# Kernel optimization log

Hardware: AMD Instinct MI355X
Metric: run time of the kernel (lower is better)

Reference implementation:

```python
import jax, jax.numpy as jnp
import numpy as np

B, S, E, H, L, D = 16, 512, 512, 8, 3, 64
OBS, ACT, NA = 128, 16, 8
KAPPAS = jnp.asarray(1.0 - 2.0 ** (-5.0 - np.arange(H)), jnp.float32)  # per-head retention decay, decay_scaling_factor=1.0
INV_SQRT_D = 1.0 / float(np.sqrt(D))


def rmsnorm(x, w, eps=1e-6):
    return x * jax.lax.rsqrt(jnp.mean(x * x, -1, keepdims=True) + eps) * w


def swiglu(x, wg, wp):
    return jax.nn.silu(x @ wg) * (x @ wp)


def sin_pe(ts, dim):
    # sinusoidal timestep positional encoding, ts: (B,S) float -> (B,S,dim)
    half = dim // 2
    freqs = jnp.exp(-np.log(10000.0) * jnp.arange(half, dtype=jnp.float32) / half)
    ang = ts[..., None] * freqs
    return jnp.concatenate([jnp.sin(ang), jnp.cos(ang)], -1)


def retention(xk, xq, xv, h0, ts, wq, wk, wv, wo, masked):
    # chunkwise multi-scale retention with cross-chunk recurrent state h0: (B,H,D,D)
    b, s, e = xq.shape
    pe = sin_pe(ts, e)
    q = ((xq + pe) @ wq).reshape(b, s, H, D).transpose(0, 2, 1, 3)            # (B,H,S,D)
    k = ((xk + pe) @ wk).reshape(b, s, H, D).transpose(0, 2, 1, 3) * INV_SQRT_D
    v = ((xv + pe) @ wv).reshape(b, s, H, D).transpose(0, 2, 1, 3)
    lk = jnp.log(KAPPAS)                                                      # (H,)
    diff = ts[:, None, :, None] - ts[:, None, None, :]                        # (B,1,S,S) timestep gaps
    if masked:
        idx = jnp.arange(s)
        allow = (diff > 0) | ((diff == 0) & (idx[:, None] >= idx[None, :]))
        dmat = jnp.where(allow, jnp.exp(lk[None, :, None, None] * diff), 0.0)
    else:
        dmat = jnp.exp(lk[None, :, None, None] * jnp.abs(diff))
    scores = jnp.einsum('bhnd,bhmd->bhnm', q, k) * dmat                       # decay-masked scores
    xi = jnp.exp(lk[None, :, None] * (ts[:, None, :] + 1.0))                  # (B,H,S) cross-chunk decay
    out = jnp.einsum('bhnm,bhmd->bhnd', scores, v) + jnp.einsum('bhnd,bhde->bhne', q, h0) * xi[..., None]
    tmax = ts.max(-1)                                                         # (B,)
    wst = jnp.exp(lk[None, :, None] * (tmax[:, None, None] - ts[:, None, :]))  # (B,H,S)
    h_new = jnp.exp(lk[None, :] * (tmax[:, None] + 1.0))[..., None, None] * h0 \
        + jnp.einsum('bhm,bhmd,bhme->bhde', wst, k, v)
    out = out.transpose(0, 2, 1, 3).reshape(b, s, e) @ wo
    return out, h_new


def _forward(obs, action, enc_hs, dec_hs1, dec_hs2, step_count, params):
    (eoln, eow, eln, ewq, ewk, ewv, ewo, eln1, eln2, efg, efp,
     ehw1, ehb1, ehln, ehw2, ehb2,
     daw, dln, dwq1, dwk1, dwv1, dwo1, dwq2, dwk2, dwv2, dwo2,
     dln1, dln2, dln3, dfg, dfp,
     dhw1, dhb1, dhln, dhw2, dhb2) = params
    ts = step_count.astype(jnp.float32)
    # ---- Encoder ----
    obs_rep = jax.nn.gelu(rmsnorm(obs, eoln) @ eow)
    enc_new = []
    for i in range(L):
        x = rmsnorm(obs_rep, eln)
        ret, hn = retention(x, x, x, enc_hs[:, i], ts, ewq[i], ewk[i], ewv[i], ewo[i], masked=False)
        x = rmsnorm(x + ret, eln1[i])
        obs_rep = rmsnorm(x + swiglu(x, efg[i], efp[i]), eln2[i])
        enc_new.append(hn)
    value = rmsnorm(jax.nn.gelu(obs_rep @ ehw1 + ehb1), ehln) @ ehw2 + ehb2
    # ---- Decoder ----
    x = rmsnorm(jax.nn.gelu(action @ daw), dln)
    d1_new, d2_new = [], []
    for i in range(L):
        ret, h1 = retention(x, x, x, dec_hs1[:, i], ts, dwq1[i], dwk1[i], dwv1[i], dwo1[i], masked=True)
        r = rmsnorm(x + ret, dln1[i])
        ret2, h2 = retention(r, obs_rep, r, dec_hs2[:, i], ts, dwq2[i], dwk2[i], dwv2[i], dwo2[i], masked=True)
        y = rmsnorm(obs_rep + ret2, dln2[i])
        x = rmsnorm(y + swiglu(y, dfg[i], dfp[i]), dln3[i])
        d1_new.append(h1)
        d2_new.append(h2)
    logits = rmsnorm(jax.nn.gelu(x @ dhw1 + dhb1), dhln) @ dhw2 + dhb2
    return value, logits, jnp.stack(enc_new, 1), jnp.stack(d1_new, 1), jnp.stack(d2_new, 1)


def setup_inputs():
    key = jax.random.key(0)
    ki = iter(jax.random.split(key, 50))
    def w(shape, s=0.02):
        return jax.random.normal(next(ki), shape, jnp.float32) * s
    inp = {
        'obs': jax.random.normal(next(ki), (B, S, OBS), jnp.float32),
        'action': jax.random.uniform(next(ki), (B, S, ACT + 1), jnp.float32),
        'enc_hs': jnp.zeros((B, L, H, D, D), jnp.float32),
        'dec_hs1': jnp.zeros((B, L, H, D, D), jnp.float32),
        'dec_hs2': jnp.zeros((B, L, H, D, D), jnp.float32),
        'step_count': jnp.broadcast_to(jnp.arange(S, dtype=jnp.int32) // NA, (B, S)),
        'enc_obs_ln_w': jnp.ones((OBS,), jnp.float32),
        'enc_obs_w': w((OBS, E)),
        'enc_ln_w': jnp.ones((E,), jnp.float32),
        'enc_wq': w((L, E, E)), 'enc_wk': w((L, E, E)), 'enc_wv': w((L, E, E)), 'enc_wo': w((L, E, E)),
        'enc_ln1_w': jnp.ones((L, E), jnp.float32), 'enc_ln2_w': jnp.ones((L, E), jnp.float32),
        'enc_ffn_gate': w((L, E, E)), 'enc_ffn_proj': w((L, E, E)),
        'enc_head_w1': w((E, E)), 'enc_head_b1': jnp.zeros((E,), jnp.float32),
        'enc_head_ln': jnp.ones((E,), jnp.float32),
        'enc_head_w2': w((E, 1)), 'enc_head_b2': jnp.zeros((1,), jnp.float32),
        'dec_act_w': w((ACT + 1, E)), 'dec_ln_w': jnp.ones((E,), jnp.float32),
        'dec_wq1': w((L, E, E)), 'dec_wk1': w((L, E, E)), 'dec_wv1': w((L, E, E)), 'dec_wo1': w((L, E, E)),
        'dec_wq2': w((L, E, E)), 'dec_wk2': w((L, E, E)), 'dec_wv2': w((L, E, E)), 'dec_wo2': w((L, E, E)),
        'dec_ln1_w': jnp.ones((L, E), jnp.float32), 'dec_ln2_w': jnp.ones((L, E), jnp.float32),
        'dec_ln3_w': jnp.ones((L, E), jnp.float32),
        'dec_ffn_gate': w((L, E, E)), 'dec_ffn_proj': w((L, E, E)),
        'dec_head_w1': w((E, E)), 'dec_head_b1': jnp.zeros((E,), jnp.float32),
        'dec_head_ln': jnp.ones((E,), jnp.float32),
        'dec_head_w2': w((E, ACT)), 'dec_head_b2': jnp.zeros((ACT,), jnp.float32),
    }
    return inp


def reference(obs, action, enc_hs, dec_hs1, dec_hs2, step_count, enc_obs_ln_w, enc_obs_w, enc_ln_w, enc_wq, enc_wk, enc_wv, enc_wo, enc_ln1_w, enc_ln2_w, enc_ffn_gate, enc_ffn_proj, enc_head_w1, enc_head_b1, enc_head_ln, enc_head_w2, enc_head_b2, dec_act_w, dec_ln_w, dec_wq1, dec_wk1, dec_wv1, dec_wo1, dec_wq2, dec_wk2, dec_wv2, dec_wo2, dec_ln1_w, dec_ln2_w, dec_ln3_w, dec_ffn_gate, dec_ffn_proj, dec_head_w1, dec_head_b1, dec_head_ln, dec_head_w2, dec_head_b2):
    params = (enc_obs_ln_w, enc_obs_w, enc_ln_w, enc_wq, enc_wk, enc_wv, enc_wo, enc_ln1_w, enc_ln2_w, enc_ffn_gate, enc_ffn_proj, enc_head_w1, enc_head_b1, enc_head_ln, enc_head_w2, enc_head_b2, dec_act_w, dec_ln_w, dec_wq1, dec_wk1, dec_wv1, dec_wo1, dec_wq2, dec_wk2, dec_wv2, dec_wo2, dec_ln1_w, dec_ln2_w, dec_ln3_w, dec_ffn_gate, dec_ffn_proj, dec_head_w1, dec_head_b1, dec_head_ln, dec_head_w2, dec_head_b2)
    return _forward(obs, action, enc_hs, dec_hs1, dec_hs2, step_count, params)
```

## Files before the change

kernel.cpp:

```cpp
#include <hip/hip_runtime.h>
#include <hip/hip_bf16.h>
#include <math.h>

typedef __attribute__((ext_vector_type(8))) short short8;
typedef __attribute__((ext_vector_type(4))) short short4v;
typedef __attribute__((ext_vector_type(4))) float f32x4;

#define BB 16
#define SS 512
#define EE 512
#define HH 8
#define DH 64
#define LL 3
#define MM (BB*SS)
#define OBSD 128
#define ACTD 17
#define INV_SQRT_D 0.125f

#define ACT_NONE 0
#define ACT_GELU 1

#define NORM_PLAIN 0
#define NORM_ADD 1

// ... 42 lines not shown
}

struct TP50 { const float* s[50]; unsigned short* d[50]; };
__global__ __launch_bounds__(256) void wtpose_batch_kernel(TP50 tp)
{
  __shared__ float t[32][33];
  const float* src = tp.s[blockIdx.z];
  unsigned short* dst = tp.d[blockIdx.z];
  const int gx = blockIdx.x, gy = blockIdx.y;
  const int tx = threadIdx.x, ty = threadIdx.y;
  #pragma unroll
  for (int i = 0; i < 4; ++i){
    int k = gx*32 + ty + i*8, n = gy*32 + tx;
    t[ty+i*8][tx] = src[(size_t)k*EE + n];
  }
  __syncthreads();
  #pragma unroll
  for (int i = 0; i < 4; ++i){
    int k = gx*32 + tx, n = gy*32 + ty + i*8;
    dst[(size_t)n*EE + k] = f2bs(t[tx][ty+i*8]);
  }
}

template<int SW>
__global__ __launch_bounds__(256) void gemm_b_kernel(
    const unsigned short* __restrict__ A, const unsigned short* __restrict__ Wt,
    const unsigned short* __restrict__ Wt2,
    const float* __restrict__ bias, float* __restrict__ C,
    unsigned short* __restrict__ Cb,
    int Kpad, float scale, int act,
    const int* __restrict__ tsi, float dsign,
    unsigned short* __restrict__ lo_n,
    unsigned short* __restrict__ swo)
{
  __shared__ unsigned short As[2][128*64];
  __shared__ unsigned short Bs[2][64*64];
  __shared__ unsigned short Bs2[SW ? 2 : 1][SW ? 64*64 : 8];
  const int bm = blockIdx.y*128, bn = blockIdx.x*64;
  const int tid = threadIdx.x, lane = tid & 63, wv = tid >> 6;
  const int wr = wv >> 1, wc = wv & 1;
  const int l16 = lane & 15, quad = lane >> 4;

  f32x4 acc[4][2], acc2[SW ? 4 : 1][SW ? 2 : 1];
  #pragma unroll
  for (int i=0;i<4;i++){ acc[i][0]=(f32x4)(0.f); acc[i][1]=(f32x4)(0.f); }
  if (SW){
    #pragma unroll
    for (int i=0;i<4;i++){ acc2[i][0]=(f32x4)(0.f); acc2[i][1]=(f32x4)(0.f); }
  }

  const int sg = lane >> 3;
  const int lg = (lane & 7) ^ sg;
  size_t aoff[4], boff[2];
  #pragma unroll
  for (int i=0;i<4;i++)
    aoff[i] = (size_t)(bm + (wv*4+i)*8 + sg)*Kpad + lg*8;
  #pragma unroll
  for (int i=0;i<2;i++)
    boff[i] = (size_t)(bn + (wv*2+i)*8 + sg)*Kpad + lg*8;

  const int swz = (l16 & 7) << 3;

  auto STAGE = [&](int buf, int t){
    const int k0 = t*64;
    #pragma unroll
    for (int i=0;i<4;i++)
      gl16(A + aoff[i] + k0, (char*)&As[buf][0] + ((wv*4+i) << 10));
    #pragma unroll
    for (int i=0;i<2;i++)
      gl16(Wt + boff[i] + k0, (char*)&Bs[buf][0] + ((wv*2+i) << 10));
    if (SW){
      #pragma unroll
      for (int i=0;i<2;i++)
        gl16(Wt2 + boff[i] + k0, (char*)&Bs2[buf][0] + ((wv*2+i) << 10));
    }
  };
  auto COMPUTE = [&](int buf){
    short8 af[4][2], bf[2][2];
    #pragma unroll
    for (int mt=0; mt<4; ++mt)
      #pragma unroll
      for (int ks=0; ks<2; ++ks)
        af[mt][ks] = *(const short8*)&As[buf][(wr*64 + mt*16 + l16)*64 + ((ks*32 + quad*8) ^ swz)];
    #pragma unroll
    for (int nt=0; nt<2; ++nt)
      #pragma unroll
      for (int ks=0; ks<2; ++ks)
        bf[nt][ks] = *(const short8*)&Bs[buf][(wc*32 + nt*16 + l16)*64 + ((ks*32 + quad*8) ^ swz)];
    #pragma unroll
    for (int ks=0; ks<2; ++ks)
      #pragma unroll
      for (int mt=0; mt<4; ++mt)
        #pragma unroll
        for (int nt=0; nt<2; ++nt)
          acc[mt][nt] = __builtin_amdgcn_mfma_f32_16x16x32_bf16(af[mt][ks], bf[nt][ks], acc[mt][nt], 0, 0, 0);
    if (SW){
      short8 bf2[2][2];
      #pragma unroll
      for (int nt=0; nt<2; ++nt)
        #pragma unroll
        for (int ks=0; ks<2; ++ks)
          bf2[nt][ks] = *(const short8*)&Bs2[buf][(wc*32 + nt*16 + l16)*64 + ((ks*32 + quad*8) ^ swz)];
      #pragma unroll
      for (int ks=0; ks<2; ++ks)
        #pragma unroll
        for (int mt=0; mt<4; ++mt)
          #pragma unroll
          for (int nt=0; nt<2; ++nt)
            acc2[mt][nt] = __builtin_amdgcn_mfma_f32_16x16x32_bf16(af[mt][ks], bf2[nt][ks], acc2[mt][nt], 0, 0, 0);
    }
  };

  const int NT = Kpad >> 6;
  STAGE(0, 0);
  PIPE_SYNC;
  int cur = 0;
  for (int t = 0; t < NT; ++t){
    if (t+1 < NT) STAGE(cur^1, t+1);
    COMPUTE(cur);
    if (t+1 < NT) PIPE_SYNC;
    cur ^= 1;
  }

  const float lkh = (!SW && tsi) ? lkappa(bn >> 6) : 0.f;
  #pragma unroll
  for (int mt=0; mt<4; ++mt){
    int rb = bm + wr*64 + mt*16 + quad*4;
    if (SW){
      #pragma unroll
      for (int nt=0; nt<2; ++nt){
        int col = bn + wc*32 + nt*16 + l16;
        #pragma unroll
        for (int j=0;j<4;j++)
          swo[(size_t)(rb+j)*EE + col] = f2bs(silu_f(acc[mt][nt][j])*acc2[mt][nt][j]);
      }
      continue;
    }
    float e0[4];
    if (tsi){
      #pragma unroll
      for (int j=0;j<4;j++) e0[j] = __expf(dsign*lkh*(float)tsi[rb+j]);
    }
    #pragma unroll
    for (int nt=0; nt<2; ++nt){
      int col = bn + wc*32 + nt*16 + l16;
      float bv = bias ? bias[col] : 0.f;
      float vals[4];
      #pragma unroll
      for (int j=0;j<4;j++){
        float v = acc[mt][nt][j]*scale + bv;
        if (act==ACT_GELU) v = gelu_f(v);
        vals[j] = v;
      }
      if (C){
        #pragma unroll
        for (int j=0;j<4;j++) C[(size_t)(rb+j)*EE + col] = vals[j];
      }
      if (Cb){
        #pragma unroll
        for (int j=0;j<4;j++) Cb[(size_t)(rb+j)*EE + col] = f2bs(vals[j]);
      }
      if (tsi){
        #pragma unroll
        for (int j=0;j<4;j++) lo_n[(size_t)(rb+j)*EE + col] = f2bs(vals[j]*e0[j]);
      }
    }
  }
}

template<int ENC>
__global__ __launch_bounds__(256) void gemm_qkv_kernel(
    const unsigned short* __restrict__ A, const unsigned short* __restrict__ Wt,
    int gstart, const int* __restrict__ tsi,
    unsigned short* __restrict__ qlo, unsigned short* __restrict__ qhi,
    unsigned short* __restrict__ klo, unsigned short* __restrict__ kloT,
    unsigned short* __restrict__ khi, unsigned short* __restrict__ khiT,
    unsigned short* __restrict__ vT)
{
  __shared__ unsigned short As[2][128*64];
  __shared__ unsigned short Bs[2][64*64];
  const int bm = blockIdx.y*128, bn = blockIdx.x*64;
  const int tid = threadIdx.x, lane = tid & 63, wv = tid >> 6;
  const int wr = wv >> 1, wc = wv & 1;
  const int l16 = lane & 15, quad = lane >> 4;

  f32x4 acc[4][2];
  #pragma unroll
  for (int i=0;i<4;i++){ acc[i][0]=(f32x4)(0.f); acc[i][1]=(f32x4)(0.f); }

  const int sg = lane >> 3;
  const int lg = (lane & 7) ^ sg;
  size_t aoff[4], boff[2];
  #pragma unroll
  for (int i=0;i<4;i++)
    aoff[i] = (size_t)(bm + (wv*4+i)*8 + sg)*EE + lg*8;
  #pragma unroll
  for (int i=0;i<2;i++)
    boff[i] = (size_t)(bn + (wv*2+i)*8 + sg)*EE + lg*8;

  const int swz = (l16 & 7) << 3;

  auto STAGE = [&](int buf, int t){
    const int k0 = t*64;
    #pragma unroll
    for (int i=0;i<4;i++)
      gl16(A + aoff[i] + k0, (char*)&As[buf][0] + ((wv*4+i) << 10));
    #pragma unroll
    for (int i=0;i<2;i++)
      gl16(Wt + boff[i] + k0, (char*)&Bs[buf][0] + ((wv*2+i) << 10));
  };
  auto COMPUTE = [&](int buf){
    short8 af[4][2], bf[2][2];
    #pragma unroll
    for (int mt=0; mt<4; ++mt)
      #pragma unroll
      for (int ks=0; ks<2; ++ks)
        af[mt][ks] = *(const short8*)&As[buf][(wr*64 + mt*16 + l16)*64 + ((ks*32 + quad*8) ^ swz)];
    #pragma unroll
    for (int nt=0; nt<2; ++nt)
      #pragma unroll
      for (int ks=0; ks<2; ++ks)
        bf[nt][ks] = *(const short8*)&Bs[buf][(wc*32 + nt*16 + l16)*64 + ((ks*32 + quad*8) ^ swz)];
    #pragma unroll
    for (int ks=0; ks<2; ++ks)
      #pragma unroll
      for (int mt=0; mt<4; ++mt)
        #pragma unroll
        for (int nt=0; nt<2; ++nt)
          acc[mt][nt] = __builtin_amdgcn_mfma_f32_16x16x32_bf16(af[mt][ks], bf[nt][ks], acc[mt][nt], 0, 0, 0);
  };

  STAGE(0, 0);
  PIPE_SYNC;
  int cur = 0;
  for (int t = 0; t < 8; ++t){
    if (t+1 < 8) STAGE(cur^1, t+1);
    COMPUTE(cur);
    if (t+1 < 8) PIPE_SYNC;
    cur ^= 1;
  }

  const int group = gstart + (bn >> 9);
  const int coll = bn & 511;
  const int hh = coll >> 6;
  const float lkh = lkappa(hh);
  const float scl = (group == 1) ? INV_SQRT_D : 1.f;
  const float dsg = (group == 1) ? -1.f : 1.f;

  #pragma unroll
  for (int mt=0; mt<4; ++mt){
    int rb = bm + wr*64 + mt*16 + quad*4;
    float e0[4], e1[4];
    if (group < 2){
      #pragma unroll
      for (int j=0;j<4;j++){
        float x = dsg*lkh*(float)tsi[rb+j];
        e0[j] = __expf(x); e1[j] = __expf(-x);
      }
    }
    int bloc = rb >> 9, m0 = rb & 511;
    #pragma unroll
    for (int nt=0; nt<2; ++nt){
      int col = coll + wc*32 + nt*16 + l16;
      int ee = col & 63;
      size_t taddr = (((size_t)bloc*HH + hh)*DH + ee)*SS + m0;
      float vals[4];
      #pragma unroll
      for (int j=0;j<4;j++) vals[j] = acc[mt][nt][j]*scl;
      if (group == 0){
        #pragma unroll
        for (int j=0;j<4;j++) qlo[(size_t)(rb+j)*EE + col] = f2bs(vals[j]*e0[j]);
        if (ENC){
          #pragma unroll
          for (int j=0;j<4;j++) qhi[(size_t)(rb+j)*EE + col] = f2bs(vals[j]*e1[j]);
        }
      } else if (group == 1){
        short4v pk;
        #pragma unroll
        for (int j=0;j<4;j++){
          unsigned short v = f2bs(vals[j]*e0[j]);
          klo[(size_t)(rb+j)*EE + col] = v;
          pk[j] = (short)v;
        }
        *(short4v*)&kloT[taddr] = pk;
        if (ENC){
          short4v pk2;
          #pragma unroll
          for (int j=0;j<4;j++){
            unsigned short v = f2bs(vals[j]*e1[j]);
            khi[(size_t)(rb+j)*EE + col] = v;
            pk2[j] = (short)v;
          }
          *(short4v*)&khiT[taddr] = pk2;
        }
      } else {
        short4v pk;
        #pragma unroll
        for (int j=0;j<4;j++) pk[j] = (short)f2bs(vals[j]);
        *(short4v*)&vT[taddr] = pk;
      }
    }
  }
}

__global__ __launch_bounds__(256) void norm_b_kernel(
    const float* __restrict__ af, const unsigned short* __restrict__ ab,
    const float* __restrict__ res, const unsigned short* __restrict__ resb,
    const float* __restrict__ w, unsigned short* __restrict__ o1,
    unsigned short* __restrict__ o2, const unsigned short* __restrict__ peb,
    int mode)
{
  const int row = blockIdx.x*4 + (threadIdx.x >> 6);
  const int lane = threadIdx.x & 63;
  const size_t base = (size_t)row*EE + lane*8;
  float t[8];
  if (ab){
    short8 av = *(const short8*)&ab[base];
    #pragma unroll
    for (int e=0;e<8;++e) t[e] = bs2f((unsigned short)av[e]);
  } else {
    float4 a0 = *(const float4*)&af[base];
    float4 a1 = *(const float4*)&af[base+4];
    t[0]=a0.x;t[1]=a0.y;t[2]=a0.z;t[3]=a0.w;t[4]=a1.x;t[5]=a1.y;t[6]=a1.z;t[7]=a1.w;
// ... 37 lines not shown
    const float* __restrict__ a, const float* __restrict__ w, unsigned short* __restrict__ o)
{
  const int row = blockIdx.x*4 + (threadIdx.x >> 6);
  const int lane = threadIdx.x & 63;
  const size_t base = (size_t)row*OBSD + lane*2;
  float2 av = *(const float2*)&a[base];
  float ss = av.x*av.x + av.y*av.y;
  #pragma unroll
  for (int off=32;off;off>>=1) ss += __shfl_xor(ss, off);
  float r = 1.f/sqrtf(ss/(float)OBSD + 1e-6f);
  float2 wv2 = *(const float2*)&w[lane*2];
  unsigned int pk = (unsigned int)f2bs(av.x*r*wv2.x) | ((unsigned int)f2bs(av.y*r*wv2.y) << 16);
  *(unsigned int*)&o[base] = pk;
}

__global__ __launch_bounds__(256) void act_embed_kernel(
    const float* __restrict__ a, unsigned short* __restrict__ o)
{
  int idx = blockIdx.x*256 + threadIdx.x;
  int row = idx >> 6, col = idx & 63;
  o[idx] = (col < ACTD) ? f2bs(a[(size_t)row*ACTD + col]) : 0;
}

__global__ __launch_bounds__(256) void wchunk_kernel(
    const unsigned short* __restrict__ kloT, const unsigned short* __restrict__ khiT,
    const unsigned short* __restrict__ vT,
    float* __restrict__ wlo, unsigned short* __restrict__ whi, int enc)
{
  __shared__ unsigned short vsh[64*72];
  __shared__ unsigned short ksh[64*72];
  __shared__ unsigned short ksh2[64*72];
  const int c = blockIdx.x, h = blockIdx.y, b = blockIdx.z;
  const int tid = threadIdx.x, lane = tid & 63, wv = tid >> 6;
  const int quad = lane >> 4, l16 = lane & 15;
  const int mc = c*64;
  {
    const int r = tid >> 2, seg = (tid & 3)*16;
    const unsigned short* vrow = vT   + (((size_t)b*HH + h)*DH + r)*SS + mc + seg;
    const unsigned short* krow = kloT + (((size_t)b*HH + h)*DH + r)*SS + mc + seg;
    #pragma unroll
    for (int i = 0; i < 2; ++i){
      *(short8*)&vsh[r*72 + seg + i*8] = *(const short8*)(vrow + i*8);
      *(short8*)&ksh[r*72 + seg + i*8] = *(const short8*)(krow + i*8);
    }
    if (enc){
      const unsigned short* k2row = khiT + (((size_t)b*HH + h)*DH + r)*SS + mc + seg;
      #pragma unroll
      for (int i = 0; i < 2; ++i)
        *(short8*)&ksh2[r*72 + seg + i*8] = *(const short8*)(k2row + i*8);
    }
  }
  __syncthreads();
  short8 av[2];
  #pragma unroll
  for (int ks=0; ks<2; ++ks)
    av[ks] = *(const short8*)&vsh[(wv*16 + l16)*72 + ks*32 + quad*8];
  f32x4 acc[4];
  #pragma unroll
  for (int dt=0; dt<4; ++dt) acc[dt] = (f32x4)(0.f);
  #pragma unroll
  for (int ks=0; ks<2; ++ks)
    #pragma unroll
    for (int dt=0; dt<4; ++dt){
      short8 kb = *(const short8*)&ksh[(dt*16 + l16)*72 + ks*32 + quad*8];
      acc[dt] = __builtin_amdgcn_mfma_f32_16x16x32_bf16(av[ks], kb, acc[dt], 0, 0, 0);
    }
  size_t obase = (((size_t)b*HH + h)*8 + c)*4096;
  #pragma unroll
  for (int dt=0; dt<4; ++dt)
    #pragma unroll
    for (int j=0;j<4;j++)
      wlo[obase + (size_t)(wv*16 + quad*4 + j)*64 + dt*16 + l16] = acc[dt][j];
  if (enc){
    f32x4 acc2[4];
    #pragma unroll
    for (int dt=0; dt<4; ++dt) acc2[dt] = (f32x4)(0.f);
    #pragma unroll
    for (int ks=0; ks<2; ++ks)
      #pragma unroll
      for (int dt=0; dt<4; ++dt){
        short8 kb = *(const short8*)&ksh2[(dt*16 + l16)*72 + ks*32 + quad*8];
        acc2[dt] = __builtin_amdgcn_mfma_f32_16x16x32_bf16(av[ks], kb, acc2[dt], 0, 0, 0);
      }
    #pragma unroll
    for (int dt=0; dt<4; ++dt)
      #pragma unroll
      for (int j=0;j<4;j++)
        whi[obase + (size_t)(wv*16 + quad*4 + j)*64 + dt*16 + l16] = f2bs(acc2[dt][j]);
  }
}

__global__ __launch_bounds__(256) void wscan_kernel(
    const float* __restrict__ wc, unsigned short* __restrict__ wcum,
    unsigned short* whi,
    const float* __restrict__ h0, const float* __restrict__ tmx,
    float* __restrict__ hnew, int enc)
{
  const int bh = blockIdx.x, b = bh >> 3, h = bh & 7;
  const float lk = lkappa(h);
  const float elk = __expf(lk);
  const float etm = __expf(lk*tmx[b]);
  const size_t wbase = (size_t)bh*8*4096;
  const size_t hbase = (size_t)b*(LL*HH*DH*DH) + (size_t)h*(DH*DH);
  for (int i = 0; i < 16; ++i){
    int p = i*256 + threadIdx.x;
    int e = p >> 6, d = p & 63;
    float acc = elk * h0[hbase + d*64 + e];
    #pragma unroll
    for (int c = 0; c < 8; ++c){
      float reg = wc[wbase + c*4096 + p];
      wcum[wbase + c*4096 + p] = f2bs(acc);
      acc += reg;
    }
    hnew[hbase + d*64 + e] = etm * acc;
    if (enc){
      float a2 = 0.f;
      #pragma unroll
      for (int c = 7; c >= 0; --c){
        float reg = bs2f(whi[wbase + c*4096 + p]);
        whi[wbase + c*4096 + p] = f2bs(a2);
        a2 += reg;
      }
    }
  }
}

template<int ENC>
__global__ __launch_bounds__(256) void retention2_kernel(
    const unsigned short* __restrict__ qlo, const unsigned short* __restrict__ qhi,
    const unsigned short* __restrict__ klo, const unsigned short* __restrict__ khi,
    const unsigned short* __restrict__ vT,
    const unsigned short* __restrict__ wlo, const unsigned short* __restrict__ whi,
    const int* __restrict__ tsi, unsigned short* __restrict__ outp)
{
  __shared__ unsigned short qsh[64*72];
  __shared__ unsigned short wsh[64*72];
  __shared__ unsigned short ksh[64*72];
  __shared__ unsigned short vsh[64*72];
  __shared__ unsigned short qsh2[ENC ? 64*72 : 2];
  __shared__ unsigned short wsh2[ENC ? 64*72 : 2];
  __shared__ float tsf[SS];
  const int b = blockIdx.z, h = blockIdx.y, t = blockIdx.x;
  const int n0 = t*64;
  const int tid = threadIdx.x, lane = tid & 63, wv = tid >> 6;
  const int quad = lane >> 4, l16 = lane & 15;
// ... 257 lines not shown
  const float* dwk1 = (const float*)d_in[25];
  const float* dwv1 = (const float*)d_in[26];
  const float* dwo1 = (const float*)d_in[27];
  const float* dwq2 = (const float*)d_in[28];
  const float* dwk2 = (const float*)d_in[29];
  const float* dwv2 = (const float*)d_in[30];
  const float* dwo2 = (const float*)d_in[31];
  const float* dln1 = (const float*)d_in[32];
  const float* dln2 = (const float*)d_in[33];
  const float* dln3 = (const float*)d_in[34];
  const float* dfg  = (const float*)d_in[35];
  const float* dfp  = (const float*)d_in[36];
  const float* dhw1 = (const float*)d_in[37];
  const float* dhb1 = (const float*)d_in[38];
  const float* dhln = (const float*)d_in[39];
  const float* dhw2 = (const float*)d_in[40];
  const float* dhb2 = (const float*)d_in[41];

  const size_t BUF = (size_t)MM*EE;
  float* wsf  = (float*)d_ws;
  float* f32a = wsf;
  float* f32b = f32a + BUF;
  float* tmx  = f32b + BUF;
  float* wc_lo = f32b;
  unsigned short* wcum_lo = (unsigned short*)f32a;
  unsigned short* wcum_hi = wcum_lo + BUF;
  unsigned short* sw_b    = (unsigned short*)f32b;
  unsigned short* ub = (unsigned short*)(tmx + 64);
  unsigned short* xrep_b    = ub;  ub += BUF;
  unsigned short* xrep_pe_b = ub;  ub += BUF;
  unsigned short* x_b       = ub;  ub += BUF;
  unsigned short* x_pe_b    = ub;  ub += BUF;
  unsigned short* t1_b      = ub;  ub += BUF;
  unsigned short* t1_pe_b   = ub;  ub += BUF;
  unsigned short* peb       = ub;  ub += BUF;
  unsigned short* qlo_b     = ub;  ub += BUF;
  unsigned short* klo_b     = ub;  ub += BUF;
  unsigned short* kloT_b    = ub;  ub += BUF;
  unsigned short* khi_b     = ub;  ub += BUF;
  unsigned short* khiT_b    = ub;  ub += BUF;
  unsigned short* vT_b      = ub;  ub += BUF;
  unsigned short* obs_n     = ub;  ub += (size_t)MM*OBSD;
  unsigned short* act_b     = obs_n;
  unsigned short* qhi_b     = t1_pe_b;
  const size_t W55 = (size_t)EE*EE;
  unsigned short* wts = ub;  ub += 50*W55;
  unsigned short* wt_eow = ub; ub += (size_t)EE*OBSD;
// ... 31 lines not shown
    for (int i=0;i<3;++i){ add(ewq+i*W55); add(ewk+i*W55); add(ewv+i*W55); }
    for (int i=0;i<3;++i) add(ewo+i*W55);
    for (int i=0;i<3;++i) add(efg+i*W55);
    for (int i=0;i<3;++i) add(efp+i*W55);
    add(ehw1);
    for (int i=0;i<3;++i){ add(dwq1+i*W55); add(dwk1+i*W55); add(dwv1+i*W55); }
    for (int i=0;i<3;++i) add(dwo1+i*W55);
    for (int i=0;i<3;++i){ add(dwk2+i*W55); add(dwv2+i*W55); }
    for (int i=0;i<3;++i) add(dwq2+i*W55);
    for (int i=0;i<3;++i) add(dwo2+i*W55);
    for (int i=0;i<3;++i) add(dfg+i*W55);
    for (int i=0;i<3;++i) add(dfp+i*W55);
    add(dhw1);
    wtpose_batch_kernel<<<dim3(16,16,50), dim3(32,8), 0, stream>>>(tp);
  }
  wtpose_kernel<<<dim3(4,16), dim3(32,8), 0, stream>>>(eow, wt_eow, OBSD, OBSD);
  wtpose_kernel<<<dim3(2,16), dim3(32,8), 0, stream>>>(daw, wt_daw, ACTD, 64);

  pe_kernel<<<(MM*EE)/256, 256, 0, stream>>>(stepc, peb);
  tsmax_kernel<<<BB, 256, 0, stream>>>(stepc, tmx);

  auto gemmF = [&](const unsigned short* A, const unsigned short* Wt, const float* bias,
                   float* C, int Kpad, float scale, int act){
    gemm_b_kernel<0><<<dim3(EE/64, MM/128), 256, 0, stream>>>(A, Wt, nullptr, bias, C, nullptr,
        Kpad, scale, act, nullptr, 0.f, nullptr, nullptr);
  };
  auto gemmQ2 = [&](const unsigned short* A, const unsigned short* Wt){
    gemm_b_kernel<0><<<dim3(EE/64, MM/128), 256, 0, stream>>>(A, Wt, nullptr, nullptr, nullptr, nullptr,
        EE, 1.f, ACT_NONE, stepc, 1.f, qlo_b, nullptr);
  };
  auto gemmSW = [&](const unsigned short* A, const unsigned short* Wg, const unsigned short* Wp){
    gemm_b_kernel<1><<<dim3(EE/64, MM/128), 256, 0, stream>>>(A, Wg, Wp, nullptr, nullptr, nullptr,
        EE, 1.f, ACT_NONE, nullptr, 0.f, nullptr, sw_b);
  };
  auto gemmQKV = [&](const unsigned short* A, const unsigned short* Wt, int enc){
    if (enc)
      gemm_qkv_kernel<1><<<dim3(24, MM/128), 256, 0, stream>>>(A, Wt, 0, stepc,
          qlo_b, qhi_b, klo_b, kloT_b, khi_b, khiT_b, vT_b);
    else
      gemm_qkv_kernel<0><<<dim3(24, MM/128), 256, 0, stream>>>(A, Wt, 0, stepc,
          qlo_b, nullptr, klo_b, kloT_b, nullptr, nullptr, vT_b);
  };
  auto gemmKV = [&](const unsigned short* A, const unsigned short* Wt){
    gemm_qkv_kernel<0><<<dim3(16, MM/128), 256, 0, stream>>>(A, Wt, 1, stepc,
        nullptr, nullptr, klo_b, kloT_b, nullptr, nullptr, vT_b);
  };
  auto norm = [&](const float* af, const unsigned short* ab, const float* res,
                  const unsigned short* resb, const float* w,
                  unsigned short* o1, unsigned short* o2, int mode){
    norm_b_kernel<<<MM/4, 256, 0, stream>>>(af, ab, res, resb, w, o1, o2, peb, mode);
  };
  auto retention = [&](const float* h0, float* hnew, unsigned short* o, int enc){
    wchunk_kernel<<<dim3(8, HH, BB), 256, 0, stream>>>(kloT_b, khiT_b, vT_b, wc_lo,
        enc ? wcum_hi : nullptr, enc);
    wscan_kernel<<<BB*HH, 256, 0, stream>>>(wc_lo, wcum_lo, enc ? wcum_hi : nullptr,
        h0, tmx, hnew, enc);
    if (enc)
      retention2_kernel<1><<<dim3(8, HH, BB), 256, 0, stream>>>(
          qlo_b, qhi_b, klo_b, khi_b, vT_b, wcum_lo, wcum_hi, stepc, o);
    else
      retention2_kernel<0><<<dim3(8, HH, BB), 256, 0, stream>>>(
          qlo_b, nullptr, klo_b, nullptr, vT_b, wcum_lo, nullptr, stepc, o);
  };

  norm_obs_kernel<<<MM/4, 256, 0, stream>>>(obs, eoln, obs_n);
  gemmF(obs_n, wt_eow, nullptr, f32a, OBSD, 1.f, ACT_GELU);

  for (int i = 0; i < LL; ++i){
    if (i == 0) norm(f32a, nullptr, nullptr, nullptr, eln, x_b, x_pe_b, NORM_PLAIN);
    else        norm(nullptr, xrep_b, nullptr, nullptr, eln, x_b, x_pe_b, NORM_PLAIN);
    gemmQKV(x_pe_b, wt_eqkv + (size_t)3*i*W55, 1);
    retention(enc_hs + i*HS_L, enc_out + i*HS_L, t1_b, 1);
    gemmF(t1_b, wt_ewo + i*W55, nullptr, f32a, EE, 1.f, ACT_NONE);
    norm(nullptr, x_b, f32a, nullptr, eln1 + i*EE, t1_b, nullptr, NORM_ADD);
    gemmSW(t1_b, wt_efg + i*W55, wt_efp + i*W55);
    norm(nullptr, t1_b, nullptr, sw_b, eln2 + i*EE, xrep_b, xrep_pe_b, NORM_ADD);
  }

  gemmF(xrep_b, wt_ehw1, ehb1, f32a, EE, 1.f, ACT_GELU);
// ... 26 lines not shown
```

Measured before the change: 1.357 ms.

## Use 128x128 GEMM tiles and fuse chunk-state computation with scan

Replaces the 128x64 GEMM kernels with a unified 128x128-tile kernel for the plain, QKV, KV and Q projections, raising operand reuse per block and halving the grid. SwiGLU gets its own kernel. The retention chunk-state GEMM and the prefix scan are merged into one kernel per (head, batch) that loops over chunks sequentially. This removes the fp32 intermediate buffer and one launch, but cuts that stage's parallelism to 128 blocks and adds per-block serial work.

Result: faster. 1.247 ms (-8.1%).

```diff
diff --git a/kernel.cpp b/kernel.cpp
--- a/kernel.cpp
+++ b/kernel.cpp
@@ -88,93 +88,67 @@
   }
 }
 
-template<int SW>
-__global__ __launch_bounds__(256) void gemm_b_kernel(
+template<int MODE, int ENC>
+__global__ __launch_bounds__(256) void gemm128_kernel(
     const unsigned short* __restrict__ A, const unsigned short* __restrict__ Wt,
-    const unsigned short* __restrict__ Wt2,
     const float* __restrict__ bias, float* __restrict__ C,
-    unsigned short* __restrict__ Cb,
     int Kpad, float scale, int act,
-    const int* __restrict__ tsi, float dsign,
-    unsigned short* __restrict__ lo_n,
-    unsigned short* __restrict__ swo)
+    int gstart, const int* __restrict__ tsi,
+    unsigned short* __restrict__ qlo, unsigned short* __restrict__ qhi,
+    unsigned short* __restrict__ klo, unsigned short* __restrict__ kloT,
+    unsigned short* __restrict__ khi, unsigned short* __restrict__ khiT,
+    unsigned short* __restrict__ vT)
 {
   __shared__ unsigned short As[2][128*64];
-  __shared__ unsigned short Bs[2][64*64];
-  __shared__ unsigned short Bs2[SW ? 2 : 1][SW ? 64*64 : 8];
-  const int bm = blockIdx.y*128, bn = blockIdx.x*64;
+  __shared__ unsigned short Bs[2][128*64];
+  const int bm = blockIdx.y*128, bn = blockIdx.x*128;
   const int tid = threadIdx.x, lane = tid & 63, wv = tid >> 6;
   const int wr = wv >> 1, wc = wv & 1;
   const int l16 = lane & 15, quad = lane >> 4;
 
-  f32x4 acc[4][2], acc2[SW ? 4 : 1][SW ? 2 : 1];
-  #pragma unroll
-  for (int i=0;i<4;i++){ acc[i][0]=(f32x4)(0.f); acc[i][1]=(f32x4)(0.f); }
-  if (SW){
-    #pragma unroll
-    for (int i=0;i<4;i++){ acc2[i][0]=(f32x4)(0.f); acc2[i][1]=(f32x4)(0.f); }
-  }
+  f32x4 acc[4][4];
+  #pragma unroll
+  for (int i=0;i<4;i++)
+    #pragma unroll
+    for (int j=0;j<4;j++) acc[i][j]=(f32x4)(0.f);
 
   const int sg = lane >> 3;
   const int lg = (lane & 7) ^ sg;
-  size_t aoff[4], boff[2];
-  #pragma unroll
-  for (int i=0;i<4;i++)
-    aoff[i] = (size_t)(bm + (wv*4+i)*8 + sg)*Kpad + lg*8;
-  #pragma unroll
-  for (int i=0;i<2;i++)
-    boff[i] = (size_t)(bn + (wv*2+i)*8 + sg)*Kpad + lg*8;
-
+  size_t aoff[4], boff[4];
+  #pragma unroll
+  for (int i=0;i<4;i++){
+    aoff[i] = (size_t)(bm + wv*32 + i*8 + sg)*Kpad + lg*8;
+    boff[i] = (size_t)(bn + wv*32 + i*8 + sg)*Kpad + lg*8;
+  }
   const int swz = (l16 & 7) << 3;
 
   auto STAGE = [&](int buf, int t){
     const int k0 = t*64;
     #pragma unroll
-    for (int i=0;i<4;i++)
+    for (int i=0;i<4;i++){
       gl16(A + aoff[i] + k0, (char*)&As[buf][0] + ((wv*4+i) << 10));
-    #pragma unroll
-    for (int i=0;i<2;i++)
-      gl16(Wt + boff[i] + k0, (char*)&Bs[buf][0] + ((wv*2+i) << 10));
-    if (SW){
-      #pragma unroll
-      for (int i=0;i<2;i++)
-        gl16(Wt2 + boff[i] + k0, (char*)&Bs2[buf][0] + ((wv*2+i) << 10));
+      gl16(Wt + boff[i] + k0, (char*)&Bs[buf][0] + ((wv*4+i) << 10));
     }
   };
   auto COMPUTE = [&](int buf){
-    short8 af[4][2], bf[2][2];
+    short8 af[4][2], bf[4][2];
     #pragma unroll
     for (int mt=0; mt<4; ++mt)
       #pragma unroll
       for (int ks=0; ks<2; ++ks)
         af[mt][ks] = *(const short8*)&As[buf][(wr*64 + mt*16 + l16)*64 + ((ks*32 + quad*8) ^ swz)];
     #pragma unroll
-    for (int nt=0; nt<2; ++nt)
+    for (int nt=0; nt<4; ++nt)
       #pragma unroll
       for (int ks=0; ks<2; ++ks)
-        bf[nt][ks] = *(const short8*)&Bs[buf][(wc*32 + nt*16 + l16)*64 + ((ks*32 + quad*8) ^ swz)];
+        bf[nt][ks] = *(const short8*)&Bs[buf][(wc*64 + nt*16 + l16)*64 + ((ks*32 + quad*8) ^ swz)];
     #pragma unroll
     for (int ks=0; ks<2; ++ks)
       #pragma unroll
       for (int mt=0; mt<4; ++mt)
         #pragma unroll
-        for (int nt=0; nt<2; ++nt)
+        for (int nt=0; nt<4; ++nt)
           acc[mt][nt] = __builtin_amdgcn_mfma_f32_16x16x32_bf16(af[mt][ks], bf[nt][ks], acc[mt][nt], 0, 0, 0);
-    if (SW){
-      short8 bf2[2][2];
-      #pragma unroll
-      for (int nt=0; nt<2; ++nt)
-        #pragma unroll
-        for (int ks=0; ks<2; ++ks)
-          bf2[nt][ks] = *(const short8*)&Bs2[buf][(wc*32 + nt*16 + l16)*64 + ((ks*32 + quad*8) ^ swz)];
-      #pragma unroll
-      for (int ks=0; ks<2; ++ks)
-        #pragma unroll
-        for (int mt=0; mt<4; ++mt)
-          #pragma unroll
-          for (int nt=0; nt<2; ++nt)
-            acc2[mt][nt] = __builtin_amdgcn_mfma_f32_16x16x32_bf16(af[mt][ks], bf2[nt][ks], acc2[mt][nt], 0, 0, 0);
-    }
   };
 
   const int NT = Kpad >> 6;
@@ -188,71 +162,103 @@
     cur ^= 1;
   }
 
-  const float lkh = (!SW && tsi) ? lkappa(bn >> 6) : 0.f;
-  #pragma unroll
-  for (int mt=0; mt<4; ++mt){
-    int rb = bm + wr*64 + mt*16 + quad*4;
-    if (SW){
-      #pragma unroll
-      for (int nt=0; nt<2; ++nt){
-        int col = bn + wc*32 + nt*16 + l16;
+  if (MODE == 0){
+    #pragma unroll
+    for (int mt=0; mt<4; ++mt){
+      int rb = bm + wr*64 + mt*16 + quad*4;
+      #pragma unroll
+      for (int nt=0; nt<4; ++nt){
+        int col = bn + wc*64 + nt*16 + l16;
+        float bv = bias ? bias[col] : 0.f;
         #pragma unroll
-        for (int j=0;j<4;j++)
-          swo[(size_t)(rb+j)*EE + col] = f2bs(silu_f(acc[mt][nt][j])*acc2[mt][nt][j]);
-      }
-      continue;
-    }
-    float e0[4];
-    if (tsi){
-      #pragma unroll
-      for (int j=0;j<4;j++) e0[j] = __expf(dsign*lkh*(float)tsi[rb+j]);
-    }
-    #pragma unroll
-    for (int nt=0; nt<2; ++nt){
-      int col = bn + wc*32 + nt*16 + l16;
-      float bv = bias ? bias[col] : 0.f;
-      float vals[4];
-      #pragma unroll
-      for (int j=0;j<4;j++){
-        float v = acc[mt][nt][j]*scale + bv;
-        if (act==ACT_GELU) v = gelu_f(v);
-        vals[j] = v;
-      }
-      if (C){
+        for (int j=0;j<4;j++){
+          float v = acc[mt][nt][j]*scale + bv;
+          if (act==ACT_GELU) v = gelu_f(v);
+          C[(size_t)(rb+j)*EE + col] = v;
+        }
+      }
+    }
+  } else {
+    const int group = gstart + (bn >> 9);
+    const int hh = ((bn & 511) >> 6) + wc;
+    const float lkh = lkappa(hh);
+    const float scl = (group == 1) ? INV_SQRT_D : 1.f;
+    const float dsg = (group == 1) ? -1.f : 1.f;
+    #pragma unroll
+    for (int mt=0; mt<4; ++mt){
+      int rb = bm + wr*64 + mt*16 + quad*4;
+      float e0[4], e1[4];
+      if (group < 2){
         #pragma unroll
-        for (int j=0;j<4;j++) C[(size_t)(rb+j)*EE + col] = vals[j];
-      }
-      if (Cb){
+        for (int j=0;j<4;j++){
+          float x = dsg*lkh*(float)tsi[rb+j];
+          e0[j] = __expf(x); e1[j] = __expf(-x);
+        }
+      }
+      int bloc = rb >> 9, m0 = rb & 511;
+      #pragma unroll
+      for (int nt=0; nt<4; ++nt){
+        int ccol = (bn & 511) + wc*64 + nt*16 + l16;
+        int ee = nt*16 + l16;
+        size_t taddr = (((size_t)bloc*HH + hh)*DH + ee)*SS + m0;
+        float vals[4];
         #pragma unroll
-        for (int j=0;j<4;j++) Cb[(size_t)(rb+j)*EE + col] = f2bs(vals[j]);
-      }
-      if (tsi){
-        #pragma unroll
-        for (int j=0;j<4;j++) lo_n[(size_t)(rb+j)*EE + col] = f2bs(vals[j]*e0[j]);
-      }
-    }
-  }
-}
-
-template<int ENC>
-__global__ __launch_bounds__(256) void gemm_qkv_kernel(
+        for (int j=0;j<4;j++) vals[j] = acc[mt][nt][j]*scl;
+        if (group == 0){
+          #pragma unroll
+          for (int j=0;j<4;j++) qlo[(size_t)(rb+j)*EE + ccol] = f2bs(vals[j]*e0[j]);
+          if (ENC){
+            #pragma unroll
+            for (int j=0;j<4;j++) qhi[(size_t)(rb+j)*EE + ccol] = f2bs(vals[j]*e1[j]);
+          }
+        } else if (group == 1){
+          short4v pk;
+          #pragma unroll
+          for (int j=0;j<4;j++){
+            unsigned short v = f2bs(vals[j]*e0[j]);
+            klo[(size_t)(rb+j)*EE + ccol] = v;
+            pk[j] = (short)v;
+          }
+          *(short4v*)&kloT[taddr] = pk;
+          if (ENC){
+            short4v pk2;
+            #pragma unroll
+            for (int j=0;j<4;j++){
+              unsigned short v = f2bs(vals[j]*e1[j]);
+              khi[(size_t)(rb+j)*EE + ccol] = v;
+              pk2[j] = (short)v;
+            }
+            *(short4v*)&khiT[taddr] = pk2;
+          }
+        } else {
+          short4v pk;
+          #pragma unroll
+          for (int j=0;j<4;j++) pk[j] = (short)f2bs(vals[j]);
+          *(short4v*)&vT[taddr] = pk;
+        }
+      }
+    }
+  }
+}
+
+__global__ __launch_bounds__(256) void gemm_sw_kernel(
     const unsigned short* __restrict__ A, const unsigned short* __restrict__ Wt,
-    int gstart, const int* __restrict__ tsi,
-    unsigned short* __restrict__ qlo, unsigned short* __restrict__ qhi,
-    unsigned short* __restrict__ klo, unsigned short* __restrict__ kloT,
-    unsigned short* __restrict__ khi, unsigned short* __restrict__ khiT,
-    unsigned short* __restrict__ vT)
+    const unsigned short* __restrict__ Wt2, unsigned short* __restrict__ swo)
 {
   __shared__ unsigned short As[2][128*64];
   __shared__ unsigned short Bs[2][64*64];
+  __shared__ unsigned short Bs2[2][64*64];
   const int bm = blockIdx.y*128, bn = blockIdx.x*64;
   const int tid = threadIdx.x, lane = tid & 63, wv = tid >> 6;
   const int wr = wv >> 1, wc = wv & 1;
   const int l16 = lane & 15, quad = lane >> 4;
 
-  f32x4 acc[4][2];
-  #pragma unroll
-  for (int i=0;i<4;i++){ acc[i][0]=(f32x4)(0.f); acc[i][1]=(f32x4)(0.f); }
+  f32x4 acc[4][2], acc2[4][2];
+  #pragma unroll
+  for (int i=0;i<4;i++){
+    acc[i][0]=(f32x4)(0.f); acc[i][1]=(f32x4)(0.f);
+    acc2[i][0]=(f32x4)(0.f); acc2[i][1]=(f32x4)(0.f);
+  }
 
   const int sg = lane >> 3;
   const int lg = (lane & 7) ^ sg;
@@ -272,11 +278,13 @@
     for (int i=0;i<4;i++)
       gl16(A + aoff[i] + k0, (char*)&As[buf][0] + ((wv*4+i) << 10));
     #pragma unroll
-    for (int i=0;i<2;i++)
+    for (int i=0;i<2;i++){
       gl16(Wt + boff[i] + k0, (char*)&Bs[buf][0] + ((wv*2+i) << 10));
+      gl16(Wt2 + boff[i] + k0, (char*)&Bs2[buf][0] + ((wv*2+i) << 10));
+    }
   };
   auto COMPUTE = [&](int buf){
-    short8 af[4][2], bf[2][2];
+    short8 af[4][2], bf[2][2], bf2[2][2];
     #pragma unroll
     for (int mt=0; mt<4; ++mt)
       #pragma unroll
@@ -285,15 +293,19 @@
     #pragma unroll
     for (int nt=0; nt<2; ++nt)
       #pragma unroll
-      for (int ks=0; ks<2; ++ks)
-        bf[nt][ks] = *(const short8*)&Bs[buf][(wc*32 + nt*16 + l16)*64 + ((ks*32 + quad*8) ^ swz)];
+      for (int ks=0; ks<2; ++ks){
+        bf[nt][ks]  = *(const short8*)&Bs[buf][(wc*32 + nt*16 + l16)*64 + ((ks*32 + quad*8) ^ swz)];
+        bf2[nt][ks] = *(const short8*)&Bs2[buf][(wc*32 + nt*16 + l16)*64 + ((ks*32 + quad*8) ^ swz)];
+      }
     #pragma unroll
     for (int ks=0; ks<2; ++ks)
       #pragma unroll
       for (int mt=0; mt<4; ++mt)
         #pragma unroll
-        for (int nt=0; nt<2; ++nt)
-          acc[mt][nt] = __builtin_amdgcn_mfma_f32_16x16x32_bf16(af[mt][ks], bf[nt][ks], acc[mt][nt], 0, 0, 0);
+        for (int nt=0; nt<2; ++nt){
+          acc[mt][nt]  = __builtin_amdgcn_mfma_f32_16x16x32_bf16(af[mt][ks], bf[nt][ks],  acc[mt][nt],  0, 0, 0);
+          acc2[mt][nt] = __builtin_amdgcn_mfma_f32_16x16x32_bf16(af[mt][ks], bf2[nt][ks], acc2[mt][nt], 0, 0, 0);
+        }
   };
 
   STAGE(0, 0);
@@ -306,65 +318,15 @@
     cur ^= 1;
   }
 
-  const int group = gstart + (bn >> 9);
-  const int coll = bn & 511;
-  const int hh = coll >> 6;
-  const float lkh = lkappa(hh);
-  const float scl = (group == 1) ? INV_SQRT_D : 1.f;
-  const float dsg = (group == 1) ? -1.f : 1.f;
-
   #pragma unroll
   for (int mt=0; mt<4; ++mt){
     int rb = bm + wr*64 + mt*16 + quad*4;
-    float e0[4], e1[4];
-    if (group < 2){
-      #pragma unroll
-      for (int j=0;j<4;j++){
-        float x = dsg*lkh*(float)tsi[rb+j];
-        e0[j] = __expf(x); e1[j] = __expf(-x);
-      }
-    }
-    int bloc = rb >> 9, m0 = rb & 511;
     #pragma unroll
     for (int nt=0; nt<2; ++nt){
-      int col = coll + wc*32 + nt*16 + l16;
-      int ee = col & 63;
-      size_t taddr = (((size_t)bloc*HH + hh)*DH + ee)*SS + m0;
-      float vals[4];
-      #pragma unroll
-      for (int j=0;j<4;j++) vals[j] = acc[mt][nt][j]*scl;
-      if (group == 0){
-        #pragma unroll
-        for (int j=0;j<4;j++) qlo[(size_t)(rb+j)*EE + col] = f2bs(vals[j]*e0[j]);
-        if (ENC){
-          #pragma unroll
-          for (int j=0;j<4;j++) qhi[(size_t)(rb+j)*EE + col] = f2bs(vals[j]*e1[j]);
-        }
-      } else if (group == 1){
-        short4v pk;
-        #pragma unroll
-        for (int j=0;j<4;j++){
-          unsigned short v = f2bs(vals[j]*e0[j]);
-          klo[(size_t)(rb+j)*EE + col] = v;
-          pk[j] = (short)v;
-        }
-        *(short4v*)&kloT[taddr] = pk;
-        if (ENC){
-          short4v pk2;
-          #pragma unroll
-          for (int j=0;j<4;j++){
-            unsigned short v = f2bs(vals[j]*e1[j]);
-            khi[(size_t)(rb+j)*EE + col] = v;
-            pk2[j] = (short)v;
-          }
-          *(short4v*)&khiT[taddr] = pk2;
-        }
-      } else {
-        short4v pk;
-        #pragma unroll
-        for (int j=0;j<4;j++) pk[j] = (short)f2bs(vals[j]);
-        *(short4v*)&vT[taddr] = pk;
-      }
+      int col = bn + wc*32 + nt*16 + l16;
+      #pragma unroll
+      for (int j=0;j<4;j++)
+        swo[(size_t)(rb+j)*EE + col] = f2bs(silu_f(acc[mt][nt][j])*acc2[mt][nt][j]);
     }
   }
 }
@@ -448,105 +410,110 @@
   o[idx] = (col < ACTD) ? f2bs(a[(size_t)row*ACTD + col]) : 0;
 }
 
-__global__ __launch_bounds__(256) void wchunk_kernel(
+__global__ __launch_bounds__(256) void wchunkscan_kernel(
     const unsigned short* __restrict__ kloT, const unsigned short* __restrict__ khiT,
     const unsigned short* __restrict__ vT,
-    float* __restrict__ wlo, unsigned short* __restrict__ whi, int enc)
+    const float* __restrict__ h0, const float* __restrict__ tmx,
+    unsigned short* __restrict__ wcum_lo, unsigned short* __restrict__ wcum_hi,
+    float* __restrict__ hnew, int enc)
 {
   __shared__ unsigned short vsh[64*72];
   __shared__ unsigned short ksh[64*72];
-  __shared__ unsigned short ksh2[64*72];
-  const int c = blockIdx.x, h = blockIdx.y, b = blockIdx.z;
+  const int h = blockIdx.x, b = blockIdx.y;
   const int tid = threadIdx.x, lane = tid & 63, wv = tid >> 6;
   const int quad = lane >> 4, l16 = lane & 15;
-  const int mc = c*64;
-  {
-    const int r = tid >> 2, seg = (tid & 3)*16;
-    const unsigned short* vrow = vT   + (((size_t)b*HH + h)*DH + r)*SS + mc + seg;
-    const unsigned short* krow = kloT + (((size_t)b*HH + h)*DH + r)*SS + mc + seg;
-    #pragma unroll
-    for (int i = 0; i < 2; ++i){
-      *(short8*)&vsh[r*72 + seg + i*8] = *(const short8*)(vrow + i*8);
-      *(short8*)&ksh[r*72 + seg + i*8] = *(const short8*)(krow + i*8);
-    }
-    if (enc){
-      const unsigned short* k2row = khiT + (((size_t)b*HH + h)*DH + r)*SS + mc + seg;
-      #pragma unroll
-      for (int i = 0; i < 2; ++i)
-        *(short8*)&ksh2[r*72 + seg + i*8] = *(const short8*)(k2row + i*8);
-    }
-  }
-  __syncthreads();
-  short8 av[2];
-  #pragma unroll
-  for (int ks=0; ks<2; ++ks)
-    av[ks] = *(const short8*)&vsh[(wv*16 + l16)*72 + ks*32 + quad*8];
-  f32x4 acc[4];
-  #pragma unroll
-  for (int dt=0; dt<4; ++dt) acc[dt] = (f32x4)(0.f);
-  #pragma unroll
-  for (int ks=0; ks<2; ++ks)
-    #pragma unroll
-    for (int dt=0; dt<4; ++dt){
-      short8 kb = *(const short8*)&ksh[(dt*16 + l16)*72 + ks*32 + quad*8];
-      acc[dt] = __builtin_amdgcn_mfma_f32_16x16x32_bf16(av[ks], kb, acc[dt], 0, 0, 0);
-    }
-  size_t obase = (((size_t)b*HH + h)*8 + c)*4096;
-  #pragma unroll
-  for (int dt=0; dt<4; ++dt)
-    #pragma unroll
-    for (int j=0;j<4;j++)
-      wlo[obase + (size_t)(wv*16 + quad*4 + j)*64 + dt*16 + l16] = acc[dt][j];
-  if (enc){
-    f32x4 acc2[4];
-    #pragma unroll
-    for (int dt=0; dt<4; ++dt) acc2[dt] = (f32x4)(0.f);
-    #pragma unroll
-    for (int ks=0; ks<2; ++ks)
-      #pragma unroll
-      for (int dt=0; dt<4; ++dt){
-        short8 kb = *(const short8*)&ksh2[(dt*16 + l16)*72 + ks*32 + quad*8];
-        acc2[dt] = __builtin_amdgcn_mfma_f32_16x16x32_bf16(av[ks], kb, acc2[dt], 0, 0, 0);
-      }
-    #pragma unroll
-    for (int dt=0; dt<4; ++dt)
-      #pragma unroll
-      for (int j=0;j<4;j++)
-        whi[obase + (size_t)(wv*16 + quad*4 + j)*64 + dt*16 + l16] = f2bs(acc2[dt][j]);
-  }
-}
-
-__global__ __launch_bounds__(256) void wscan_kernel(
-    const float* __restrict__ wc, unsigned short* __restrict__ wcum,
-    unsigned short* whi,
-    const float* __restrict__ h0, const float* __restrict__ tmx,
-    float* __restrict__ hnew, int enc)
-{
-  const int bh = blockIdx.x, b = bh >> 3, h = bh & 7;
   const float lk = lkappa(h);
   const float elk = __expf(lk);
   const float etm = __expf(lk*tmx[b]);
-  const size_t wbase = (size_t)bh*8*4096;
+  const size_t wbase = ((size_t)b*HH + h)*8*4096;
   const size_t hbase = (size_t)b*(LL*HH*DH*DH) + (size_t)h*(DH*DH);
-  for (int i = 0; i < 16; ++i){
-    int p = i*256 + threadIdx.x;
-    int e = p >> 6, d = p & 63;
-    float acc = elk * h0[hbase + d*64 + e];
-    #pragma unroll
-    for (int c = 0; c < 8; ++c){
-      float reg = wc[wbase + c*4096 + p];
-      wcum[wbase + c*4096 + p] = f2bs(acc);
-      acc += reg;
-    }
-    hnew[hbase + d*64 + e] = etm * acc;
-    if (enc){
-      float a2 = 0.f;
-      #pragma unroll
-      for (int c = 7; c >= 0; --c){
-        float reg = bs2f(whi[wbase + c*4096 + p]);
-        whi[wbase + c*4096 + p] = f2bs(a2);
-        a2 += reg;
-      }
+  const int e0r = wv*16 + quad*4;
+  const int sr = tid >> 2, sseg = (tid & 3)*16;
+
+  f32x4 cum[4];
+  #pragma unroll
+  for (int dt=0; dt<4; ++dt)
+    #pragma unroll
+    for (int j=0;j<4;j++)
+      cum[dt][j] = elk * h0[hbase + (size_t)(dt*16+l16)*64 + e0r + j];
+
+  for (int c = 0; c < 8; ++c){
+    __syncthreads();
+    {
+      const unsigned short* vrow = vT   + (((size_t)b*HH + h)*DH + sr)*SS + c*64 + sseg;
+      const unsigned short* krow = kloT + (((size_t)b*HH + h)*DH + sr)*SS + c*64 + sseg;
+      #pragma unroll
+      for (int i = 0; i < 2; ++i){
+        *(short8*)&vsh[sr*72 + sseg + i*8] = *(const short8*)(vrow + i*8);
+        *(short8*)&ksh[sr*72 + sseg + i*8] = *(const short8*)(krow + i*8);
+      }
+    }
+    __syncthreads();
+    short8 av[2];
+    #pragma unroll
+    for (int ks=0; ks<2; ++ks)
+      av[ks] = *(const short8*)&vsh[(wv*16 + l16)*72 + ks*32 + quad*8];
+    f32x4 acc[4];
+    #pragma unroll
+    for (int dt=0; dt<4; ++dt) acc[dt] = (f32x4)(0.f);
+    #pragma unroll
+    for (int ks=0; ks<2; ++ks)
+      #pragma unroll
+      for (int dt=0; dt<4; ++dt){
+        short8 kb = *(const short8*)&ksh[(dt*16 + l16)*72 + ks*32 + quad*8];
+        acc[dt] = __builtin_amdgcn_mfma_f32_16x16x32_bf16(av[ks], kb, acc[dt], 0, 0, 0);
+      }
+    #pragma unroll
+    for (int dt=0; dt<4; ++dt)
+      #pragma unroll
+      for (int j=0;j<4;j++){
+        wcum_lo[wbase + (size_t)c*4096 + (size_t)(e0r+j)*64 + dt*16 + l16] = f2bs(cum[dt][j]);
+        cum[dt][j] += acc[dt][j];
+      }
+  }
+  #pragma unroll
+  for (int dt=0; dt<4; ++dt)
+    #pragma unroll
+    for (int j=0;j<4;j++)
+      hnew[hbase + (size_t)(dt*16+l16)*64 + e0r + j] = etm * cum[dt][j];
+
+  if (enc){
+    f32x4 suf[4];
+    #pragma unroll
+    for (int dt=0; dt<4; ++dt) suf[dt] = (f32x4)(0.f);
+    for (int c = 7; c >= 0; --c){
+      __syncthreads();
+      {
+        const unsigned short* vrow = vT   + (((size_t)b*HH + h)*DH + sr)*SS + c*64 + sseg;
+        const unsigned short* krow = khiT + (((size_t)b*HH + h)*DH + sr)*SS + c*64 + sseg;
+        #pragma unroll
+        for (int i = 0; i < 2; ++i){
+          *(short8*)&vsh[sr*72 + sseg + i*8] = *(const short8*)(vrow + i*8);
+          *(short8*)&ksh[sr*72 + sseg + i*8] = *(const short8*)(krow + i*8);
+        }
+      }
+      __syncthreads();
+      short8 av[2];
+      #pragma unroll
+      for (int ks=0; ks<2; ++ks)
+        av[ks] = *(const short8*)&vsh[(wv*16 + l16)*72 + ks*32 + quad*8];
+      f32x4 acc[4];
+      #pragma unroll
+      for (int dt=0; dt<4; ++dt) acc[dt] = (f32x4)(0.f);
+      #pragma unroll
+      for (int ks=0; ks<2; ++ks)
+        #pragma unroll
+        for (int dt=0; dt<4; ++dt){
+          short8 kb = *(const short8*)&ksh[(dt*16 + l16)*72 + ks*32 + quad*8];
+          acc[dt] = __builtin_amdgcn_mfma_f32_16x16x32_bf16(av[ks], kb, acc[dt], 0, 0, 0);
+        }
+      #pragma unroll
+      for (int dt=0; dt<4; ++dt)
+        #pragma unroll
+        for (int j=0;j<4;j++){
+          wcum_hi[wbase + (size_t)c*4096 + (size_t)(e0r+j)*64 + dt*16 + l16] = f2bs(suf[dt][j]);
+          suf[dt][j] += acc[dt][j];
+        }
     }
   }
 }
@@ -850,7 +817,6 @@
   float* f32a = wsf;
   float* f32b = f32a + BUF;
   float* tmx  = f32b + BUF;
-  float* wc_lo = f32b;
   unsigned short* wcum_lo = (unsigned short*)f32a;
   unsigned short* wcum_hi = wcum_lo + BUF;
   unsigned short* sw_b    = (unsigned short*)f32b;
@@ -928,28 +894,32 @@
 
   auto gemmF = [&](const unsigned short* A, const unsigned short* Wt, const float* bias,
                    float* C, int Kpad, float scale, int act){
-    gemm_b_kernel<0><<<dim3(EE/64, MM/128), 256, 0, stream>>>(A, Wt, nullptr, bias, C, nullptr,
-        Kpad, scale, act, nullptr, 0.f, nullptr, nullptr);
-  };
-  auto gemmQ2 = [&](const unsigned short* A, const unsigned short* Wt){
-    gemm_b_kernel<0><<<dim3(EE/64, MM/128), 256, 0, stream>>>(A, Wt, nullptr, nullptr, nullptr, nullptr,
-        EE, 1.f, ACT_NONE, stepc, 1.f, qlo_b, nullptr);
-  };
-  auto gemmSW = [&](const unsigned short* A, const unsigned short* Wg, const unsigned short* Wp){
-    gemm_b_kernel<1><<<dim3(EE/64, MM/128), 256, 0, stream>>>(A, Wg, Wp, nullptr, nullptr, nullptr,
-        EE, 1.f, ACT_NONE, nullptr, 0.f, nullptr, sw_b);
+    gemm128_kernel<0,0><<<dim3(EE/128, MM/128), 256, 0, stream>>>(A, Wt, bias, C,
+        Kpad, scale, act, 0, nullptr,
+        nullptr, nullptr, nullptr, nullptr, nullptr, nullptr, nullptr);
   };
   auto gemmQKV = [&](const unsigned short* A, const unsigned short* Wt, int enc){
     if (enc)
-      gemm_qkv_kernel<1><<<dim3(24, MM/128), 256, 0, stream>>>(A, Wt, 0, stepc,
+      gemm128_kernel<1,1><<<dim3(12, MM/128), 256, 0, stream>>>(A, Wt, nullptr, nullptr,
+          EE, 1.f, ACT_NONE, 0, stepc,
           qlo_b, qhi_b, klo_b, kloT_b, khi_b, khiT_b, vT_b);
     else
-      gemm_qkv_kernel<0><<<dim3(24, MM/128), 256, 0, stream>>>(A, Wt, 0, stepc,
+      gemm128_kernel<1,0><<<dim3(12, MM/128), 256, 0, stream>>>(A, Wt, nullptr, nullptr,
+          EE, 1.f, ACT_NONE, 0, stepc,
           qlo_b, nullptr, klo_b, kloT_b, nullptr, nullptr, vT_b);
   };
   auto gemmKV = [&](const unsigned short* A, const unsigned short* Wt){
-    gemm_qkv_kernel<0><<<dim3(16, MM/128), 256, 0, stream>>>(A, Wt, 1, stepc,
+    gemm128_kernel<1,0><<<dim3(8, MM/128), 256, 0, stream>>>(A, Wt, nullptr, nullptr,
+        EE, 1.f, ACT_NONE, 1, stepc,
         nullptr, nullptr, klo_b, kloT_b, nullptr, nullptr, vT_b);
+  };
+  auto gemmQ2 = [&](const unsigned short* A, const unsigned short* Wt){
+    gemm128_kernel<1,0><<<dim3(4, MM/128), 256, 0, stream>>>(A, Wt, nullptr, nullptr,
+        EE, 1.f, ACT_NONE, 0, stepc,
+        qlo_b, nullptr, nullptr, nullptr, nullptr, nullptr, nullptr);
+  };
+  auto gemmSW = [&](const unsigned short* A, const unsigned short* Wg, const unsigned short* Wp){
+    gemm_sw_kernel<<<dim3(EE/64, MM/128), 256, 0, stream>>>(A, Wg, Wp, sw_b);
   };
   auto norm = [&](const float* af, const unsigned short* ab, const float* res,
                   const unsigned short* resb, const float* w,
@@ -957,10 +927,8 @@
     norm_b_kernel<<<MM/4, 256, 0, stream>>>(af, ab, res, resb, w, o1, o2, peb, mode);
   };
   auto retention = [&](const float* h0, float* hnew, unsigned short* o, int enc){
-    wchunk_kernel<<<dim3(8, HH, BB), 256, 0, stream>>>(kloT_b, khiT_b, vT_b, wc_lo,
-        enc ? wcum_hi : nullptr, enc);
-    wscan_kernel<<<BB*HH, 256, 0, stream>>>(wc_lo, wcum_lo, enc ? wcum_hi : nullptr,
-        h0, tmx, hnew, enc);
+    wchunkscan_kernel<<<dim3(HH, BB), 256, 0, stream>>>(kloT_b, khiT_b, vT_b,
+        h0, tmx, wcum_lo, enc ? wcum_hi : wcum_lo, hnew, enc);
     if (enc)
       retention2_kernel<1><<<dim3(8, HH, BB), 256, 0, stream>>>(
           qlo_b, qhi_b, klo_b, khi_b, vT_b, wcum_lo, wcum_hi, stepc, o);
```
